# Performance work log

Hardware: AMD Instinct MI355X
Metric: run time of the kernel (lower is better)

Reference implementation:

```python
import jax, jax.numpy as jnp
import numpy as np

DIM = 1024
HEADS = 16
EPS = 1e-5  # torch nn.LayerNorm default


def layernorm(x, g, b):
    # normalize over last axis
    mu = jnp.mean(x, axis=-1, keepdims=True)
    var = jnp.mean(jnp.square(x - mu), axis=-1, keepdims=True)
    return (x - mu) * jax.lax.rsqrt(var + EPS) * g + b


def setup_inputs() -> dict:
    key = jax.random.key(0)
    ks = jax.random.split(key, 8)
    B, N, C = 4, 1024, DIM
    s = 1.0 / np.sqrt(C)
    return {
        "x": jax.random.normal(ks[0], (B, N, C), jnp.float32),
        "qkv_w": jax.random.normal(ks[1], (3 * C, C), jnp.float32) * s,
        "qkv_b": jnp.zeros((3 * C,), jnp.float32),
        "q_norm_g": jnp.ones((C,), jnp.float32),
        "q_norm_b": jnp.zeros((C,), jnp.float32),
        "k_norm_g": jnp.ones((C,), jnp.float32),
        "k_norm_b": jnp.zeros((C,), jnp.float32),
        "proj_w": jax.random.normal(ks[2], (C, C), jnp.float32) * s,
        "proj_b": jnp.zeros((C,), jnp.float32),
    }


def reference(x, qkv_w, qkv_b, q_norm_g, q_norm_b, k_norm_g, k_norm_b, proj_w, proj_b):
    B, N, C = x.shape
    H = HEADS
    D = C // H
    scale = D ** -0.5

    qkv = x @ qkv_w.T + qkv_b                      # [B,N,3C]
    qkv = qkv.reshape(B, N, 3, H, D)
    q, k, v = qkv[:, :, 0], qkv[:, :, 1], qkv[:, :, 2]  # [B,N,H,D]

    # qk_normalization: LayerNorm over flattened (H*D)=C per token
    q = layernorm(q.reshape(B, N, C), q_norm_g, q_norm_b).reshape(B, N, H, D)
    k = layernorm(k.reshape(B, N, C), k_norm_g, k_norm_b).reshape(B, N, H, D)

    # attention: [B,H,N,N]
    attn = jnp.einsum('bqhd,bkhd->bhqk', q * scale, k)
    attn = jax.nn.softmax(attn, axis=-1)
    out = jnp.einsum('bhqk,bkhd->bqhd', attn, v).reshape(B, N, C)
    return out @ proj_w.T + proj_b
```

## Files before the change

kernel.cpp:

```cpp
#include <hip/hip_runtime.h>
#include <hip/hip_bf16.h>

#define C_DIM 1024
#define HEADS 16

typedef __bf16 bf16x8 __attribute__((ext_vector_type(8)));
typedef float f32x4 __attribute__((ext_vector_type(4)));

static __device__ __forceinline__ unsigned short f2bf(float f) {
  unsigned int u = __builtin_bit_cast(unsigned int, f);
  u += 0x7FFFu + ((u >> 16) & 1u);
  return (unsigned short)(u >> 16);
}

static __device__ __forceinline__ float bf2f(unsigned short u) {
  unsigned int v = ((unsigned int)u) << 16;
  return __builtin_bit_cast(float, v);
}

static __device__ __forceinline__ void glds16(const unsigned short* g,
                                              unsigned short* l) {
  __builtin_amdgcn_global_load_lds(
      (const __attribute__((address_space(1))) unsigned int*)g,
      (__attribute__((address_space(3))) unsigned int*)l, 16, 0, 0);
}

__global__ void cast_bf16_kernel(const float* __restrict__ src,
                                 unsigned short* __restrict__ dst, int n4) {
  int i = blockIdx.x * blockDim.x + threadIdx.x;
  if (i >= n4) return;
  float4 v = *reinterpret_cast<const float4*>(src + (size_t)i * 4);
  ushort4 o;
  o.x = f2bf(v.x); o.y = f2bf(v.y); o.z = f2bf(v.z); o.w = f2bf(v.w);
  *reinterpret_cast<ushort4*>(dst + (size_t)i * 4) = o;
}

__global__ void cast2_kernel(const float* __restrict__ s0,
                             const float* __restrict__ s1,
                             unsigned short* __restrict__ d0,
                             unsigned short* __restrict__ d1, int n40) {
  int i = blockIdx.x * 256 + threadIdx.x;
  const float* s;
  unsigned short* d;
  if (i < n40) { s = s0; d = d0; }
  else { s = s1; d = d1; i -= n40; }
  float4 v = *reinterpret_cast<const float4*>(s + (size_t)i * 4);
  ushort4 o;
  o.x = f2bf(v.x); o.y = f2bf(v.y); o.z = f2bf(v.z); o.w = f2bf(v.w);
  *reinterpret_cast<ushort4*>(d + (size_t)i * 4) = o;
}

template <bool BF16_OUT>
__global__ __launch_bounds__(256, 2) void gemm_nt(
    const unsigned short* __restrict__ A, const unsigned short* __restrict__ B,
    const float* __restrict__ bias, void* __restrict__ Cout,
    int M, int N, int K) {
  __shared__ __align__(16) unsigned short As[128 * 64];
  __shared__ __align__(16) unsigned short Bs[128 * 64];
  const int tid = threadIdx.x;
  const int lane = tid & 63;
  const int wave = tid >> 6;
  const int wm = wave >> 1, wn = wave & 1;
  const int g = lane >> 4, r = lane & 15;
  const int bm = blockIdx.x * 128, bn = blockIdx.y * 128;

  f32x4 acc[4][4] = {};

  for (int k0 = 0; k0 < K; k0 += 64) {
    __syncthreads();
#pragma unroll
    for (int i = 0; i < 4; ++i) {
      int cb = i * 256 + wave * 64;
      int c = cb + lane;
      int row = c >> 3, col = (c & 7) * 8;
      glds16(&A[(size_t)(bm + row) * K + k0 + col], &As[cb * 8]);
      glds16(&B[(size_t)(bn + row) * K + k0 + col], &Bs[cb * 8]);
    }
    __syncthreads();

    bf16x8 af[4][2], bf[4][2];
#pragma unroll
    for (int m = 0; m < 4; ++m) {
      af[m][0] = *reinterpret_cast<const bf16x8*>(&As[(wm * 64 + m * 16 + r) * 64 + g * 8]);
      af[m][1] = *reinterpret_cast<const bf16x8*>(&As[(wm * 64 + m * 16 + r) * 64 + 32 + g * 8]);
    }
#pragma unroll
    for (int n = 0; n < 4; ++n) {
      bf[n][0] = *reinterpret_cast<const bf16x8*>(&Bs[(wn * 64 + n * 16 + r) * 64 + g * 8]);
      bf[n][1] = *reinterpret_cast<const bf16x8*>(&Bs[(wn * 64 + n * 16 + r) * 64 + 32 + g * 8]);
    }
#pragma unroll
    for (int m = 0; m < 4; ++m)
#pragma unroll
      for (int n = 0; n < 4; ++n) {
        acc[m][n] = __builtin_amdgcn_mfma_f32_16x16x32_bf16(af[m][0], bf[n][0], acc[m][n], 0, 0, 0);
        acc[m][n] = __builtin_amdgcn_mfma_f32_16x16x32_bf16(af[m][1], bf[n][1], acc[m][n], 0, 0, 0);
      }
  }

#pragma unroll
  for (int m = 0; m < 4; ++m) {
    int row0 = bm + wm * 64 + m * 16 + g * 4;
#pragma unroll
    for (int n = 0; n < 4; ++n) {
      int col = bn + wn * 64 + n * 16 + r;
      float bv = bias[col];
#pragma unroll
      for (int rr = 0; rr < 4; ++rr) {
        float v = acc[m][n][rr] + bv;
        if (BF16_OUT)
          reinterpret_cast<unsigned short*>(Cout)[(size_t)(row0 + rr) * N + col] = f2bf(v);
        else
          reinterpret_cast<float*>(Cout)[(size_t)(row0 + rr) * N + col] = v;
      }
    }
  }
}

__global__ __launch_bounds__(256) void ln_pack_kernel(
    const unsigned short* __restrict__ qkv, const float* __restrict__ qg,
    const float* __restrict__ qb, const float* __restrict__ kg,
    const float* __restrict__ kb, unsigned short* __restrict__ Q,
    unsigned short* __restrict__ Ko) {
  const int t = blockIdx.x;
  const int b = t >> 10, n = t & 1023;
  const int tid = threadIdx.x;
  const int lane = tid & 63, wave = tid >> 6;
  const unsigned short* row = qkv + (size_t)t * 3072;
  ushort4 qu = *reinterpret_cast<const ushort4*>(row + tid * 4);
  ushort4 ku = *reinterpret_cast<const ushort4*>(row + 1024 + tid * 4);
  float q0 = bf2f(qu.x), q1 = bf2f(qu.y), q2 = bf2f(qu.z), q3 = bf2f(qu.w);
  float k0 = bf2f(ku.x), k1 = bf2f(ku.y), k2 = bf2f(ku.z), k3 = bf2f(ku.w);

  float qs = q0 + q1 + q2 + q3;
  float qss = q0 * q0 + q1 * q1 + q2 * q2 + q3 * q3;
  float ks = k0 + k1 + k2 + k3;
  float kss = k0 * k0 + k1 * k1 + k2 * k2 + k3 * k3;
#pragma unroll
  for (int m = 1; m < 64; m <<= 1) {
    qs += __shfl_xor(qs, m);
    qss += __shfl_xor(qss, m);
    ks += __shfl_xor(ks, m);
    kss += __shfl_xor(kss, m);
  }
  __shared__ float red[4][4];
  if (lane == 0) {
    red[wave][0] = qs; red[wave][1] = qss; red[wave][2] = ks; red[wave][3] = kss;
  }
  __syncthreads();
  qs = red[0][0] + red[1][0] + red[2][0] + red[3][0];
  qss = red[0][1] + red[1][1] + red[2][1] + red[3][1];
  ks = red[0][2] + red[1][2] + red[2][2] + red[3][2];
  kss = red[0][3] + red[1][3] + red[2][3] + red[3][3];
  const float inv = 1.0f / 1024.0f;
  float qmu = qs * inv, kmu = ks * inv;
  float qrs = rsqrtf(qss * inv - qmu * qmu + 1e-5f);
  float krs = rsqrtf(kss * inv - kmu * kmu + 1e-5f);

  int c0 = tid * 4;
  float4 qg4 = *reinterpret_cast<const float4*>(qg + c0);
  float4 qb4 = *reinterpret_cast<const float4*>(qb + c0);
  float4 kg4 = *reinterpret_cast<const float4*>(kg + c0);
  float4 kb4 = *reinterpret_cast<const float4*>(kb + c0);
  int h = c0 >> 6, d = c0 & 63;
  size_t off = (((size_t)(b * HEADS + h)) * 1024 + n) * 64 + d;
  ushort4 qo, ko;
  const float QS = 0.125f * 1.44269504f;
  qo.x = f2bf(((q0 - qmu) * qrs * qg4.x + qb4.x) * QS);
  qo.y = f2bf(((q1 - qmu) * qrs * qg4.y + qb4.y) * QS);
  qo.z = f2bf(((q2 - qmu) * qrs * qg4.z + qb4.z) * QS);
  qo.w = f2bf(((q3 - qmu) * qrs * qg4.w + qb4.w) * QS);
  ko.x = f2bf((k0 - kmu) * krs * kg4.x + kb4.x);
  ko.y = f2bf((k1 - kmu) * krs * kg4.y + kb4.y);
  ko.z = f2bf((k2 - kmu) * krs * kg4.z + kb4.z);
  ko.w = f2bf((k3 - kmu) * krs * kg4.w + kb4.w);
  *reinterpret_cast<ushort4*>(Q + off) = qo;
  *reinterpret_cast<ushort4*>(Ko + off) = ko;
}

__global__ __launch_bounds__(256) void transpose_v(
    const unsigned short* __restrict__ qkv, unsigned short* __restrict__ VT) {
  const int bid = blockIdx.x;
  const int bh = bid >> 4, nt = bid & 15;
  const int b = bh >> 4, h = bh & 15;
  unsigned short* dst = VT + (size_t)bh * 65536 + nt * 64;
  __shared__ __align__(16) unsigned short tile[64][68];
  const int tid = threadIdx.x;
#pragma unroll
  for (int i = 0; i < 4; ++i) {
    int idx = i * 256 + tid;
    int row = idx >> 4, c4 = (idx & 15) * 4;
    int t = b * 1024 + nt * 64 + row;
    *reinterpret_cast<ushort4*>(&tile[row][c4]) =
        *reinterpret_cast<const ushort4*>(&qkv[(size_t)t * 3072 + 2048 + h * 64 + c4]);
  }
  __syncthreads();
#pragma unroll
  for (int i = 0; i < 4; ++i) {
    int idx = i * 256 + tid;
    int d = idx >> 4, p = (idx & 15) * 4;
    int key0 = 16 * (2 * (p >> 5) + ((p >> 2) & 1)) + 4 * ((p >> 3) & 3);
    ushort4 o;
    o.x = tile[key0][d]; o.y = tile[key0 + 1][d];
    o.z = tile[key0 + 2][d]; o.w = tile[key0 + 3][d];
    *reinterpret_cast<ushort4*>(&dst[(size_t)d * 1024 + p]) = o;
  }
}

__global__ __launch_bounds__(256, 4) void attn_kernel(
    const unsigned short* __restrict__ Q, const unsigned short* __restrict__ K,
    const unsigned short* __restrict__ VT, unsigned short* __restrict__ O) {
  const int blk = blockIdx.x;
  const int bh = blk & 63;
  const int qb = blk >> 6;
  const int tid = threadIdx.x;
  const int lane = tid & 63, wave = tid >> 6;
  const int g = lane >> 4, r = lane & 15;
  const unsigned short* Qh = Q + (size_t)bh * 65536;
  const unsigned short* Kh = K + (size_t)bh * 65536;
  const unsigned short* Vth = VT + (size_t)bh * 65536;
  const int q0 = qb * 64 + wave * 16;

  __shared__ __align__(16) unsigned short KL[2][4096];
  __shared__ __align__(16) unsigned short VL[2][4096];

  bf16x8 bq0 = *reinterpret_cast<const bf16x8*>(&Qh[(q0 + r) * 64 + g * 8]);
  bf16x8 bq1 = *reinterpret_cast<const bf16x8*>(&Qh[(q0 + r) * 64 + 32 + g * 8]);

  f32x4 ao[4] = {};
  float mreg = -1e30f, lreg = 0.f;

  auto STAGE = [&](int b, int kt) {
#pragma unroll
    for (int t = 0; t < 2; ++t) {
      int cb = (wave * 2 + t) * 64;
      int i = cb + lane;
      int row = i >> 3, pcol = i & 7;
      int lc = pcol ^ (row & 7);
      glds16(Kh + (size_t)(kt + row) * 64 + lc * 8, &KL[b][cb * 8]);
      glds16(Vth + (size_t)row * 1024 + kt + lc * 8, &VL[b][cb * 8]);
    }
  };

  STAGE(0, 0);
  __syncthreads();
  int cur = 0;

  for (int kt = 0; kt < 1024; kt += 64) {
    if (kt + 64 < 1024) STAGE(cur ^ 1, kt + 64);
    const unsigned short* KB = KL[cur];
    const unsigned short* VB = VL[cur];
    const int sw = r & 7;

    f32x4 s[4];
#pragma unroll
    for (int j = 0; j < 4; ++j) {
      const int row = 16 * j + r;
      bf16x8 k0 = *reinterpret_cast<const bf16x8*>(&KB[row * 64 + (g ^ sw) * 8]);
      bf16x8 k1 = *reinterpret_cast<const bf16x8*>(&KB[row * 64 + ((4 + g) ^ sw) * 8]);
      f32x4 t = {};
      t = __builtin_amdgcn_mfma_f32_16x16x32_bf16(k0, bq0, t, 0, 0, 0);
      t = __builtin_amdgcn_mfma_f32_16x16x32_bf16(k1, bq1, t, 0, 0, 0);
      s[j] = t;
    }
    float a0 = fmaxf(fmaxf(s[0][0], s[0][1]), s[0][2]);
    float a1 = fmaxf(fmaxf(s[0][3], s[1][0]), s[1][1]);
    float a2 = fmaxf(fmaxf(s[1][2], s[1][3]), s[2][0]);
    float a3 = fmaxf(fmaxf(s[2][1], s[2][2]), s[2][3]);
    float a4 = fmaxf(fmaxf(s[3][0], s[3][1]), s[3][2]);
    float v = fmaxf(fmaxf(fmaxf(a0, a1), fmaxf(a2, a3)), fmaxf(a4, s[3][3]));
    v = fmaxf(v, __shfl_xor(v, 16));
    v = fmaxf(v, __shfl_xor(v, 32));
    if (!__all((int)(v - mreg <= 8.0f))) {
      float mnew = fmaxf(mreg, v);
      float fac = exp2f(mreg - mnew);
      mreg = mnew;
      lreg *= fac;
      float facr[4];
#pragma unroll
      for (int rr = 0; rr < 4; ++rr)
        facr[rr] = __shfl(fac, (lane & 48) | (4 * g + rr));
#pragma unroll
      for (int n = 0; n < 4; ++n)
#pragma unroll
        for (int rr = 0; rr < 4; ++rr) ao[n][rr] *= facr[rr];
    }
#pragma unroll
    for (int j = 0; j < 4; ++j)
#pragma unroll
      for (int rr = 0; rr < 4; ++rr) s[j][rr] = exp2f(s[j][rr] - mreg);
    float ps = ((s[0][0] + s[0][1]) + (s[0][2] + s[0][3])) +
               ((s[1][0] + s[1][1]) + (s[1][2] + s[1][3])) +
               ((s[2][0] + s[2][1]) + (s[2][2] + s[2][3])) +
               ((s[3][0] + s[3][1]) + (s[3][2] + s[3][3]));
    ps += __shfl_xor(ps, 16);
    ps += __shfl_xor(ps, 32);
    lreg += ps;
    uint4 u0, u1;
    asm("v_cvt_pk_bf16_f32 %0, %1, %2" : "=v"(u0.x) : "v"(s[0][0]), "v"(s[0][1]));
    asm("v_cvt_pk_bf16_f32 %0, %1, %2" : "=v"(u0.y) : "v"(s[0][2]), "v"(s[0][3]));
    asm("v_cvt_pk_bf16_f32 %0, %1, %2" : "=v"(u0.z) : "v"(s[1][0]), "v"(s[1][1]));
    asm("v_cvt_pk_bf16_f32 %0, %1, %2" : "=v"(u0.w) : "v"(s[1][2]), "v"(s[1][3]));
    asm("v_cvt_pk_bf16_f32 %0, %1, %2" : "=v"(u1.x) : "v"(s[2][0]), "v"(s[2][1]));
    asm("v_cvt_pk_bf16_f32 %0, %1, %2" : "=v"(u1.y) : "v"(s[2][2]), "v"(s[2][3]));
    asm("v_cvt_pk_bf16_f32 %0, %1, %2" : "=v"(u1.z) : "v"(s[3][0]), "v"(s[3][1]));
    asm("v_cvt_pk_bf16_f32 %0, %1, %2" : "=v"(u1.w) : "v"(s[3][2]), "v"(s[3][3]));
    bf16x8 ap0 = __builtin_bit_cast(bf16x8, u0);
    bf16x8 ap1 = __builtin_bit_cast(bf16x8, u1);
#pragma unroll
    for (int n = 0; n < 4; ++n) {
      const int row = n * 16 + r;
      bf16x8 v0 = *reinterpret_cast<const bf16x8*>(&VB[row * 64 + (g ^ sw) * 8]);
      bf16x8 v1 = *reinterpret_cast<const bf16x8*>(&VB[row * 64 + ((4 + g) ^ sw) * 8]);
      ao[n] = __builtin_amdgcn_mfma_f32_16x16x32_bf16(ap0, v0, ao[n], 0, 0, 0);
      ao[n] = __builtin_amdgcn_mfma_f32_16x16x32_bf16(ap1, v1, ao[n], 0, 0, 0);
    }
    __syncthreads();
    cur ^= 1;
  }

  const int b = bh >> 4, h = bh & 15;
  float lr[4];
#pragma unroll
  for (int rr = 0; rr < 4; ++rr)
    lr[rr] = 1.0f / __shfl(lreg, (lane & 48) | (4 * g + rr));
#pragma unroll
  for (int n = 0; n < 4; ++n)
#pragma unroll
    for (int rr = 0; rr < 4; ++rr) {
      int tok = q0 + 4 * g + rr;
      O[(((size_t)(b * 1024 + tok)) * 16 + h) * 64 + n * 16 + r] =
          f2bf(ao[n][rr] * lr[rr]);
    }
}

__global__ void sentinel_kernel(unsigned short* out, float v) {
  if (threadIdx.x == 0 && blockIdx.x == 0) out[0] = f2bf(v);
}

extern "C" void kernel_launch(void* const* d_in, const int* in_sizes, int n_in,
                              void* d_out, int out_size, void* d_ws, size_t ws_size,
                              hipStream_t stream) {
  const float* x      = (const float*)d_in[0];
  const float* qkv_w  = (const float*)d_in[1];
  const float* qkv_b  = (const float*)d_in[2];
  const float* q_g    = (const float*)d_in[3];
  const float* q_b    = (const float*)d_in[4];
  const float* k_g    = (const float*)d_in[5];
  const float* k_b    = (const float*)d_in[6];
  const float* proj_w = (const float*)d_in[7];
  const float* proj_b = (const float*)d_in[8];

  const int M = in_sizes[0] / C_DIM;
  const int Bb = M / 1024;

  const size_t required = (size_t)M * 3072 * 2 + (size_t)3 * M * 1024 * 2;
  if (ws_size < required) {
    sentinel_kernel<<<1, 64, 0, stream>>>((unsigned short*)d_out, (float)ws_size);
    return;
  }

  unsigned short* qkv_bf = (unsigned short*)d_ws;
  unsigned short* Qb = qkv_bf + (size_t)M * 3072;
  unsigned short* Kb = Qb + (size_t)M * 1024;
  unsigned short* VTn = Kb + (size_t)M * 1024;
  unsigned short* x_bf = Qb;
  unsigned short* qw_bf = Kb;
  unsigned short* AO = qkv_bf;
  unsigned short* pw_bf = qkv_bf + (size_t)2 * M * 1024;

  const int n4x = M * 1024 / 4;
  const int n4w1 = 3072 * 1024 / 4;
  const int n4w2 = 1024 * 1024 / 4;
  cast2_kernel<<<(n4x + n4w1) / 256, 256, 0, stream>>>(
      x, qkv_w, x_bf, qw_bf, n4x);

  gemm_nt<true><<<dim3(M / 128, 3072 / 128), 256, 0, stream>>>(
      x_bf, qw_bf, qkv_b, qkv_bf, M, 3072, 1024);

  ln_pack_kernel<<<M, 256, 0, stream>>>(qkv_bf, q_g, q_b, k_g, k_b, Qb, Kb);

  transpose_v<<<Bb * HEADS * 16, 256, 0, stream>>>(qkv_bf, VTn);

  cast_bf16_kernel<<<n4w2 / 256, 256, 0, stream>>>(proj_w, pw_bf, n4w2);

  attn_kernel<<<Bb * HEADS * 16, 256, 0, stream>>>(Qb, Kb, VTn, AO);

  gemm_nt<false><<<dim3(M / 128, 1024 / 128), 256, 0, stream>>>(
      AO, pw_bf, proj_b, (float*)d_out, M, 1024, 1024);
}
```

Baseline: 123.9 us.

## Merge LN and V-transpose launches, fold proj cast into attention, drop LDS staging

Combines the LayerNorm-pack and V-transpose kernels into one launch split by block index. The proj weight cast is folded into extra blocks of the attention launch, cutting total launches from six to four. The attention kernel also drops its double-buffered LDS staging of K and V^T and loads MFMA operands straight from global memory into registers, with no block barriers. This removes launch gaps and LDS/sync overhead, but each wave now reads K and V independently, relying on cache instead of shared reuse, with less latency hiding.

```diff
diff --git a/kernel.cpp b/kernel.cpp
--- a/kernel.cpp
+++ b/kernel.cpp
@@ -23,16 +23,6 @@
   __builtin_amdgcn_global_load_lds(
       (const __attribute__((address_space(1))) unsigned int*)g,
       (__attribute__((address_space(3))) unsigned int*)l, 16, 0, 0);
-}
-
-__global__ void cast_bf16_kernel(const float* __restrict__ src,
-                                 unsigned short* __restrict__ dst, int n4) {
-  int i = blockIdx.x * blockDim.x + threadIdx.x;
-  if (i >= n4) return;
-  float4 v = *reinterpret_cast<const float4*>(src + (size_t)i * 4);
-  ushort4 o;
-  o.x = f2bf(v.x); o.y = f2bf(v.y); o.z = f2bf(v.z); o.w = f2bf(v.w);
-  *reinterpret_cast<ushort4*>(dst + (size_t)i * 4) = o;
 }
 
 __global__ void cast2_kernel(const float* __restrict__ s0,
@@ -117,100 +107,110 @@
   }
 }
 
-__global__ __launch_bounds__(256) void ln_pack_kernel(
+__global__ __launch_bounds__(256) void prep_kernel(
     const unsigned short* __restrict__ qkv, const float* __restrict__ qg,
     const float* __restrict__ qb, const float* __restrict__ kg,
     const float* __restrict__ kb, unsigned short* __restrict__ Q,
-    unsigned short* __restrict__ Ko) {
-  const int t = blockIdx.x;
-  const int b = t >> 10, n = t & 1023;
+    unsigned short* __restrict__ Ko, unsigned short* __restrict__ VT,
+    int nLN) {
+  __shared__ __align__(16) unsigned short tile[64][68];
+  __shared__ float red[4][4];
+  const int bid = blockIdx.x;
   const int tid = threadIdx.x;
-  const int lane = tid & 63, wave = tid >> 6;
-  const unsigned short* row = qkv + (size_t)t * 3072;
-  ushort4 qu = *reinterpret_cast<const ushort4*>(row + tid * 4);
-  ushort4 ku = *reinterpret_cast<const ushort4*>(row + 1024 + tid * 4);
-  float q0 = bf2f(qu.x), q1 = bf2f(qu.y), q2 = bf2f(qu.z), q3 = bf2f(qu.w);
-  float k0 = bf2f(ku.x), k1 = bf2f(ku.y), k2 = bf2f(ku.z), k3 = bf2f(ku.w);
-
-  float qs = q0 + q1 + q2 + q3;
-  float qss = q0 * q0 + q1 * q1 + q2 * q2 + q3 * q3;
-  float ks = k0 + k1 + k2 + k3;
-  float kss = k0 * k0 + k1 * k1 + k2 * k2 + k3 * k3;
-#pragma unroll
-  for (int m = 1; m < 64; m <<= 1) {
-    qs += __shfl_xor(qs, m);
-    qss += __shfl_xor(qss, m);
-    ks += __shfl_xor(ks, m);
-    kss += __shfl_xor(kss, m);
-  }
-  __shared__ float red[4][4];
-  if (lane == 0) {
-    red[wave][0] = qs; red[wave][1] = qss; red[wave][2] = ks; red[wave][3] = kss;
-  }
-  __syncthreads();
-  qs = red[0][0] + red[1][0] + red[2][0] + red[3][0];
-  qss = red[0][1] + red[1][1] + red[2][1] + red[3][1];
-  ks = red[0][2] + red[1][2] + red[2][2] + red[3][2];
-  kss = red[0][3] + red[1][3] + red[2][3] + red[3][3];
-  const float inv = 1.0f / 1024.0f;
-  float qmu = qs * inv, kmu = ks * inv;
-  float qrs = rsqrtf(qss * inv - qmu * qmu + 1e-5f);
-  float krs = rsqrtf(kss * inv - kmu * kmu + 1e-5f);
-
-  int c0 = tid * 4;
-  float4 qg4 = *reinterpret_cast<const float4*>(qg + c0);
-  float4 qb4 = *reinterpret_cast<const float4*>(qb + c0);
-  float4 kg4 = *reinterpret_cast<const float4*>(kg + c0);
-  float4 kb4 = *reinterpret_cast<const float4*>(kb + c0);
-  int h = c0 >> 6, d = c0 & 63;
-  size_t off = (((size_t)(b * HEADS + h)) * 1024 + n) * 64 + d;
-  ushort4 qo, ko;
-  const float QS = 0.125f * 1.44269504f;
-  qo.x = f2bf(((q0 - qmu) * qrs * qg4.x + qb4.x) * QS);
-  qo.y = f2bf(((q1 - qmu) * qrs * qg4.y + qb4.y) * QS);
-  qo.z = f2bf(((q2 - qmu) * qrs * qg4.z + qb4.z) * QS);
-  qo.w = f2bf(((q3 - qmu) * qrs * qg4.w + qb4.w) * QS);
-  ko.x = f2bf((k0 - kmu) * krs * kg4.x + kb4.x);
-  ko.y = f2bf((k1 - kmu) * krs * kg4.y + kb4.y);
-  ko.z = f2bf((k2 - kmu) * krs * kg4.z + kb4.z);
-  ko.w = f2bf((k3 - kmu) * krs * kg4.w + kb4.w);
-  *reinterpret_cast<ushort4*>(Q + off) = qo;
-  *reinterpret_cast<ushort4*>(Ko + off) = ko;
-}
-
-__global__ __launch_bounds__(256) void transpose_v(
-    const unsigned short* __restrict__ qkv, unsigned short* __restrict__ VT) {
-  const int bid = blockIdx.x;
-  const int bh = bid >> 4, nt = bid & 15;
-  const int b = bh >> 4, h = bh & 15;
-  unsigned short* dst = VT + (size_t)bh * 65536 + nt * 64;
-  __shared__ __align__(16) unsigned short tile[64][68];
-  const int tid = threadIdx.x;
-#pragma unroll
-  for (int i = 0; i < 4; ++i) {
-    int idx = i * 256 + tid;
-    int row = idx >> 4, c4 = (idx & 15) * 4;
-    int t = b * 1024 + nt * 64 + row;
-    *reinterpret_cast<ushort4*>(&tile[row][c4]) =
-        *reinterpret_cast<const ushort4*>(&qkv[(size_t)t * 3072 + 2048 + h * 64 + c4]);
-  }
-  __syncthreads();
-#pragma unroll
-  for (int i = 0; i < 4; ++i) {
-    int idx = i * 256 + tid;
-    int d = idx >> 4, p = (idx & 15) * 4;
-    int key0 = 16 * (2 * (p >> 5) + ((p >> 2) & 1)) + 4 * ((p >> 3) & 3);
-    ushort4 o;
-    o.x = tile[key0][d]; o.y = tile[key0 + 1][d];
-    o.z = tile[key0 + 2][d]; o.w = tile[key0 + 3][d];
-    *reinterpret_cast<ushort4*>(&dst[(size_t)d * 1024 + p]) = o;
+
+  if (bid < nLN) {
+    const int t = bid;
+    const int b = t >> 10, n = t & 1023;
+    const int lane = tid & 63, wave = tid >> 6;
+    const unsigned short* row = qkv + (size_t)t * 3072;
+    ushort4 qu = *reinterpret_cast<const ushort4*>(row + tid * 4);
+    ushort4 ku = *reinterpret_cast<const ushort4*>(row + 1024 + tid * 4);
+    float q0 = bf2f(qu.x), q1 = bf2f(qu.y), q2 = bf2f(qu.z), q3 = bf2f(qu.w);
+    float k0 = bf2f(ku.x), k1 = bf2f(ku.y), k2 = bf2f(ku.z), k3 = bf2f(ku.w);
+
+    float qs = q0 + q1 + q2 + q3;
+    float qss = q0 * q0 + q1 * q1 + q2 * q2 + q3 * q3;
+    float ks = k0 + k1 + k2 + k3;
+    float kss = k0 * k0 + k1 * k1 + k2 * k2 + k3 * k3;
+#pragma unroll
+    for (int m = 1; m < 64; m <<= 1) {
+      qs += __shfl_xor(qs, m);
+      qss += __shfl_xor(qss, m);
+      ks += __shfl_xor(ks, m);
+      kss += __shfl_xor(kss, m);
+    }
+    if (lane == 0) {
+      red[wave][0] = qs; red[wave][1] = qss; red[wave][2] = ks; red[wave][3] = kss;
+    }
+    __syncthreads();
+    qs = red[0][0] + red[1][0] + red[2][0] + red[3][0];
+    qss = red[0][1] + red[1][1] + red[2][1] + red[3][1];
+    ks = red[0][2] + red[1][2] + red[2][2] + red[3][2];
+    kss = red[0][3] + red[1][3] + red[2][3] + red[3][3];
+    const float inv = 1.0f / 1024.0f;
+    float qmu = qs * inv, kmu = ks * inv;
+    float qrs = rsqrtf(qss * inv - qmu * qmu + 1e-5f);
+    float krs = rsqrtf(kss * inv - kmu * kmu + 1e-5f);
+
+    int c0 = tid * 4;
+    float4 qg4 = *reinterpret_cast<const float4*>(qg + c0);
+    float4 qb4 = *reinterpret_cast<const float4*>(qb + c0);
+    float4 kg4 = *reinterpret_cast<const float4*>(kg + c0);
+    float4 kb4 = *reinterpret_cast<const float4*>(kb + c0);
+    int h = c0 >> 6, d = c0 & 63;
+    size_t off = (((size_t)(b * HEADS + h)) * 1024 + n) * 64 + d;
+    ushort4 qo, ko;
+    const float QS = 0.125f * 1.44269504f;
+    qo.x = f2bf(((q0 - qmu) * qrs * qg4.x + qb4.x) * QS);
+    qo.y = f2bf(((q1 - qmu) * qrs * qg4.y + qb4.y) * QS);
+    qo.z = f2bf(((q2 - qmu) * qrs * qg4.z + qb4.z) * QS);
+    qo.w = f2bf(((q3 - qmu) * qrs * qg4.w + qb4.w) * QS);
+    ko.x = f2bf((k0 - kmu) * krs * kg4.x + kb4.x);
+    ko.y = f2bf((k1 - kmu) * krs * kg4.y + kb4.y);
+    ko.z = f2bf((k2 - kmu) * krs * kg4.z + kb4.z);
+    ko.w = f2bf((k3 - kmu) * krs * kg4.w + kb4.w);
+    *reinterpret_cast<ushort4*>(Q + off) = qo;
+    *reinterpret_cast<ushort4*>(Ko + off) = ko;
+  } else {
+    const int idx0 = bid - nLN;
+    const int bh = idx0 >> 4, nt = idx0 & 15;
+    const int b = bh >> 4, h = bh & 15;
+    unsigned short* dst = VT + (size_t)bh * 65536 + nt * 64;
+#pragma unroll
+    for (int i = 0; i < 4; ++i) {
+      int idx = i * 256 + tid;
+      int row = idx >> 4, c4 = (idx & 15) * 4;
+      int t = b * 1024 + nt * 64 + row;
+      *reinterpret_cast<ushort4*>(&tile[row][c4]) =
+          *reinterpret_cast<const ushort4*>(&qkv[(size_t)t * 3072 + 2048 + h * 64 + c4]);
+    }
+    __syncthreads();
+#pragma unroll
+    for (int i = 0; i < 4; ++i) {
+      int idx = i * 256 + tid;
+      int d = idx >> 4, p = (idx & 15) * 4;
+      int key0 = 16 * (2 * (p >> 5) + ((p >> 2) & 1)) + 4 * ((p >> 3) & 3);
+      ushort4 o;
+      o.x = tile[key0][d]; o.y = tile[key0 + 1][d];
+      o.z = tile[key0 + 2][d]; o.w = tile[key0 + 3][d];
+      *reinterpret_cast<ushort4*>(&dst[(size_t)d * 1024 + p]) = o;
+    }
   }
 }
 
 __global__ __launch_bounds__(256, 4) void attn_kernel(
     const unsigned short* __restrict__ Q, const unsigned short* __restrict__ K,
-    const unsigned short* __restrict__ VT, unsigned short* __restrict__ O) {
+    const unsigned short* __restrict__ VT, unsigned short* __restrict__ O,
+    int nAttn, const float* __restrict__ pw, unsigned short* __restrict__ pwb) {
   const int blk = blockIdx.x;
+  if (blk >= nAttn) {
+    int i = (blk - nAttn) * 256 + threadIdx.x;
+    float4 v = *reinterpret_cast<const float4*>(pw + (size_t)i * 4);
+    ushort4 o;
+    o.x = f2bf(v.x); o.y = f2bf(v.y); o.z = f2bf(v.z); o.w = f2bf(v.w);
+    *reinterpret_cast<ushort4*>(pwb + (size_t)i * 4) = o;
+    return;
+  }
   const int bh = blk & 63;
   const int qb = blk >> 6;
   const int tid = threadIdx.x;
@@ -221,47 +221,31 @@
   const unsigned short* Vth = VT + (size_t)bh * 65536;
   const int q0 = qb * 64 + wave * 16;
 
-  __shared__ __align__(16) unsigned short KL[2][4096];
-  __shared__ __align__(16) unsigned short VL[2][4096];
-
   bf16x8 bq0 = *reinterpret_cast<const bf16x8*>(&Qh[(q0 + r) * 64 + g * 8]);
   bf16x8 bq1 = *reinterpret_cast<const bf16x8*>(&Qh[(q0 + r) * 64 + 32 + g * 8]);
 
   f32x4 ao[4] = {};
   float mreg = -1e30f, lreg = 0.f;
 
-  auto STAGE = [&](int b, int kt) {
-#pragma unroll
-    for (int t = 0; t < 2; ++t) {
-      int cb = (wave * 2 + t) * 64;
-      int i = cb + lane;
-      int row = i >> 3, pcol = i & 7;
-      int lc = pcol ^ (row & 7);
-      glds16(Kh + (size_t)(kt + row) * 64 + lc * 8, &KL[b][cb * 8]);
-      glds16(Vth + (size_t)row * 1024 + kt + lc * 8, &VL[b][cb * 8]);
-    }
-  };
-
-  STAGE(0, 0);
-  __syncthreads();
-  int cur = 0;
+  const unsigned short* kbase = Kh + r * 64 + g * 8;
+  const unsigned short* vbase = Vth + (size_t)r * 1024 + g * 8;
 
   for (int kt = 0; kt < 1024; kt += 64) {
-    if (kt + 64 < 1024) STAGE(cur ^ 1, kt + 64);
-    const unsigned short* KB = KL[cur];
-    const unsigned short* VB = VL[cur];
-    const int sw = r & 7;
-
     f32x4 s[4];
 #pragma unroll
     for (int j = 0; j < 4; ++j) {
-      const int row = 16 * j + r;
-      bf16x8 k0 = *reinterpret_cast<const bf16x8*>(&KB[row * 64 + (g ^ sw) * 8]);
-      bf16x8 k1 = *reinterpret_cast<const bf16x8*>(&KB[row * 64 + ((4 + g) ^ sw) * 8]);
+      bf16x8 k0 = *reinterpret_cast<const bf16x8*>(kbase + (size_t)(kt + 16 * j) * 64);
+      bf16x8 k1 = *reinterpret_cast<const bf16x8*>(kbase + (size_t)(kt + 16 * j) * 64 + 32);
       f32x4 t = {};
       t = __builtin_amdgcn_mfma_f32_16x16x32_bf16(k0, bq0, t, 0, 0, 0);
       t = __builtin_amdgcn_mfma_f32_16x16x32_bf16(k1, bq1, t, 0, 0, 0);
       s[j] = t;
+    }
+    bf16x8 vb0[4], vb1[4];
+#pragma unroll
+    for (int n = 0; n < 4; ++n) {
+      vb0[n] = *reinterpret_cast<const bf16x8*>(vbase + (size_t)n * 16384 + kt);
+      vb1[n] = *reinterpret_cast<const bf16x8*>(vbase + (size_t)n * 16384 + kt + 32);
     }
     float a0 = fmaxf(fmaxf(s[0][0], s[0][1]), s[0][2]);
     float a1 = fmaxf(fmaxf(s[0][3], s[1][0]), s[1][1]);
@@ -309,14 +293,9 @@
     bf16x8 ap1 = __builtin_bit_cast(bf16x8, u1);
 #pragma unroll
     for (int n = 0; n < 4; ++n) {
-      const int row = n * 16 + r;
-      bf16x8 v0 = *reinterpret_cast<const bf16x8*>(&VB[row * 64 + (g ^ sw) * 8]);
-      bf16x8 v1 = *reinterpret_cast<const bf16x8*>(&VB[row * 64 + ((4 + g) ^ sw) * 8]);
-      ao[n] = __builtin_amdgcn_mfma_f32_16x16x32_bf16(ap0, v0, ao[n], 0, 0, 0);
-      ao[n] = __builtin_amdgcn_mfma_f32_16x16x32_bf16(ap1, v1, ao[n], 0, 0, 0);
-    }
-    __syncthreads();
-    cur ^= 1;
+      ao[n] = __builtin_amdgcn_mfma_f32_16x16x32_bf16(ap0, vb0[n], ao[n], 0, 0, 0);
+      ao[n] = __builtin_amdgcn_mfma_f32_16x16x32_bf16(ap1, vb1[n], ao[n], 0, 0, 0);
+    }
   }
 
   const int b = bh >> 4, h = bh & 15;
@@ -372,19 +351,19 @@
   const int n4x = M * 1024 / 4;
   const int n4w1 = 3072 * 1024 / 4;
   const int n4w2 = 1024 * 1024 / 4;
+
   cast2_kernel<<<(n4x + n4w1) / 256, 256, 0, stream>>>(
       x, qkv_w, x_bf, qw_bf, n4x);
 
   gemm_nt<true><<<dim3(M / 128, 3072 / 128), 256, 0, stream>>>(
       x_bf, qw_bf, qkv_b, qkv_bf, M, 3072, 1024);
 
-  ln_pack_kernel<<<M, 256, 0, stream>>>(qkv_bf, q_g, q_b, k_g, k_b, Qb, Kb);
-
-  transpose_v<<<Bb * HEADS * 16, 256, 0, stream>>>(qkv_bf, VTn);
-
-  cast_bf16_kernel<<<n4w2 / 256, 256, 0, stream>>>(proj_w, pw_bf, n4w2);
-
-  attn_kernel<<<Bb * HEADS * 16, 256, 0, stream>>>(Qb, Kb, VTn, AO);
+  prep_kernel<<<M + Bb * HEADS * 16, 256, 0, stream>>>(
+      qkv_bf, q_g, q_b, k_g, k_b, Qb, Kb, VTn, M);
+
+  const int nAttn = Bb * HEADS * 16;
+  attn_kernel<<<nAttn + n4w2 / 256, 256, 0, stream>>>(
+      Qb, Kb, VTn, AO, nAttn, proj_w, pw_bf);
 
   gemm_nt<false><<<dim3(M / 128, 1024 / 128), 256, 0, stream>>>(
       AO, pw_bf, proj_b, (float*)d_out, M, 1024, 1024);
```

Result: slower. 195.6 us (+57.8%).
